# Kernel optimization log

Hardware: AMD Instinct MI355X
Metric: run time of the kernel (lower is better)

The kernel has to match this reference:

```python
import jax, jax.numpy as jnp
import numpy as np

D = 512
F = 2048
H = 8
L = 128
B = 4


def _layer_norm(x, g, b, eps=1e-5):
    mu = jnp.mean(x, axis=-1, keepdims=True)
    var = jnp.var(x, axis=-1, keepdims=True)
    return (x - mu) * jax.lax.rsqrt(var + eps) * g + b


def _edge_mlp(Q, arc, W, b, arc_is_middle_out):
    # Equivalent to relu(Linear(concat(A, arc, B_))) with W: (3D, D), without
    # materializing the (B,L,L,3D) concat: split W into three D-blocks.
    # For W_out: concat(h_bf, arc, h_bf_t) -> block1 acts on Q[b,i], block3 on Q[b,j].
    # For W_in:  concat(h_bf_t, arc, h_bf) -> block1 acts on Q[b,j], block3 on Q[b,i].
    d = Q.shape[-1]
    W1, W2, W3 = W[:d], W[d:2 * d], W[2 * d:]
    mid = jnp.einsum('bijd,de->bije', arc, W2)
    if arc_is_middle_out:  # W_out ordering
        left = jnp.einsum('bid,de->bie', Q, W1)[:, :, None, :]   # broadcast over j
        right = jnp.einsum('bjd,de->bje', Q, W3)[:, None, :, :]  # broadcast over i
    else:  # W_in ordering
        left = jnp.einsum('bjd,de->bje', Q, W1)[:, None, :, :]
        right = jnp.einsum('bid,de->bie', Q, W3)[:, :, None, :]
    return jax.nn.relu(left + mid + right + b)


def _gat_attn(Q, KV, q_w, q_b, k_w, k_b, v_w, v_b, o_w, o_b):
    # Edge-conditioned multihead attention: per-query K/V of shape (B,L,L,D).
    bsz, seq, d = Q.shape
    dh = d // H
    scale = dh ** -0.5
    q = ((Q @ q_w + q_b) * scale).reshape(bsz, seq, H, dh)
    k = (KV @ k_w + k_b).reshape(bsz, seq, seq, H, dh)
    v = (KV @ v_w + v_b).reshape(bsz, seq, seq, H, dh)
    scores = jnp.einsum('bihd,bijhd->bhij', q, k)
    attn = jax.nn.softmax(scores, axis=-1)
    out = jnp.einsum('bhij,bijhd->bihd', attn, v).reshape(bsz, seq, d)
    return out @ o_w + o_b


def setup_inputs() -> dict:
    key = jax.random.key(0)
    ks = jax.random.split(key, 24)
    s = 0.02
    inp = {
        'h': jax.random.normal(ks[0], (L, B, D), jnp.float32),
        'src_outcoming_arc_x': jax.random.normal(ks[1], (B, L, L, D), jnp.float32),
        'src_incoming_arc_x': jax.random.normal(ks[2], (B, L, L, D), jnp.float32),
        'encoder_padding_mask': jnp.zeros((B, L), jnp.bool_),
        'W_out_w': jax.random.normal(ks[3], (3 * D, D), jnp.float32) * s,
        'W_out_b': jnp.zeros((D,), jnp.float32),
        'W_in_w': jax.random.normal(ks[4], (3 * D, D), jnp.float32) * s,
        'W_in_b': jnp.zeros((D,), jnp.float32),
        'q_w': jax.random.normal(ks[5], (D, D), jnp.float32) * s,
        'q_b': jnp.zeros((D,), jnp.float32),
        'k_w': jax.random.normal(ks[6], (D, D), jnp.float32) * s,
        'k_b': jnp.zeros((D,), jnp.float32),
        'v_w': jax.random.normal(ks[7], (D, D), jnp.float32) * s,
        'v_b': jnp.zeros((D,), jnp.float32),
        'o_w': jax.random.normal(ks[8], (D, D), jnp.float32) * s,
        'o_b': jnp.zeros((D,), jnp.float32),
        'ln1_g': jnp.ones((D,), jnp.float32),
        'ln1_b': jnp.zeros((D,), jnp.float32),
        'fc1_w': jax.random.normal(ks[9], (D, F), jnp.float32) * s,
        'fc1_b': jnp.zeros((F,), jnp.float32),
        'fc2_w': jax.random.normal(ks[10], (F, D), jnp.float32) * s,
        'fc2_b': jnp.zeros((D,), jnp.float32),
        'ln2_g': jnp.ones((D,), jnp.float32),
        'ln2_b': jnp.zeros((D,), jnp.float32),
    }
    return inp


def reference(h, src_outcoming_arc_x, src_incoming_arc_x, encoder_padding_mask,
              W_out_w, W_out_b, W_in_w, W_in_b,
              q_w, q_b, k_w, k_b, v_w, v_b, o_w, o_b,
              ln1_g, ln1_b, fc1_w, fc1_b, fc2_w, fc2_b, ln2_g, ln2_b):
    # h: (L, B, D). Dropouts are identity (eval). attn_mask=None.
    residual = h
    Q = jnp.transpose(h, (1, 0, 2))  # (B, L, D)
    U_out = _edge_mlp(Q, src_outcoming_arc_x, W_out_w, W_out_b, True)
    att_out = _gat_attn(Q, U_out, q_w, q_b, k_w, k_b, v_w, v_b, o_w, o_b)
    U_in = _edge_mlp(Q, src_incoming_arc_x, W_in_w, W_in_b, False)
    att_in = _gat_attn(Q, U_in, q_w, q_b, k_w, k_b, v_w, v_b, o_w, o_b)
    x = jnp.transpose(att_in + att_out, (1, 0, 2))  # back to (L, B, D)
    x = _layer_norm(residual + x, ln1_g, ln1_b)
    residual = x
    x = jax.nn.relu(x @ fc1_w + fc1_b) @ fc2_w + fc2_b
    x = _layer_norm(residual + x, ln2_g, ln2_b)
    return x
```

## Files before the change

### kernel.cpp

```cpp
#include <hip/hip_runtime.h>
#include <stdint.h>
#include <stddef.h>

#define NTOK 512
#define NM   65536

typedef __bf16 bf16x8 __attribute__((ext_vector_type(8)));
typedef float  f32x4  __attribute__((ext_vector_type(4)));
typedef unsigned int u32x4 __attribute__((ext_vector_type(4)));

__device__ __forceinline__ unsigned short f2bf(float f) {
    unsigned int u = __builtin_bit_cast(unsigned int, f);
    u += 0x7FFFu + ((u >> 16) & 1u);
    return (unsigned short)(u >> 16);
}
__device__ __forceinline__ float bf2f(unsigned short s) {
    unsigned int u = ((unsigned int)s) << 16;
    return __builtin_bit_cast(float, u);
}

__device__ __forceinline__ void gload16(const void* g, void* l) {
    __builtin_amdgcn_global_load_lds(
        (const __attribute__((address_space(1))) void*)g,
        (__attribute__((address_space(3))) void*)l,
        16, 0, 0);
}

__global__ __launch_bounds__(256) void k_prep(const float* __restrict__ h,
                                              unsigned short* __restrict__ Qm,
                                              const float* __restrict__ kw,
                                              float* __restrict__ kwT,
                                              const float* __restrict__ Wob,
                                              const float* __restrict__ Wib,
                                              const float* __restrict__ qb,
                                              float* __restrict__ bias1) {
    int bid = blockIdx.x;
    int t = threadIdx.x;
    if (bid < 1024) {
        int idx = bid * 256 + t;
        int tok = idx >> 9, d = idx & 511;
        int b = tok >> 7, i = tok & 127;
        Qm[idx] = f2bf(h[(i * 4 + b) * 512 + d]);
    } else if (bid < 2048) {
        int idx = (bid - 1024) * 256 + t;
        kwT[idx] = kw[(size_t)(idx & 511) * 512 + (idx >> 9)];
    } else {
        int i = (bid - 2048) * 256 + t;
        if (i < 2560) {
            float v = 0.f;
            if (i < 512) v = Wob[i];
            else if (i < 1024) v = 0.f;
            else if (i < 1536) v = Wib[i - 1024];
            else if (i < 2048) v = 0.f;
            else v = qb[i - 2048] * 0.125f;
            bias1[i] = v;
        }
    }
}

struct TRJob { const float* src; unsigned short* dst; int srcLd, dstLd, tcols; float scale; };
struct TRJobs { TRJob j[11]; int start[12]; };

__global__ __launch_bounds__(256) void k_trN(TRJobs js) {
    __shared__ float tile[64][65];
    int b = blockIdx.x;
    int ji = 0;
    while (ji < 10 && b >= js.start[ji + 1]) ++ji;
    TRJob jb = js.j[ji];
    int rel = b - js.start[ji];
    int bx = rel % jb.tcols, by = rel / jb.tcols;
    int r0 = by * 64, c0 = bx * 64;
    int t = threadIdx.x;
    int c = t & 63, rr = t >> 6;
    #pragma unroll
    for (int ii = 0; ii < 16; ++ii) {
        int r = ii * 4 + rr;
        tile[r][c] = jb.src[(size_t)(r0 + r) * jb.srcLd + c0 + c];
    }
    __syncthreads();
    #pragma unroll
    for (int ii = 0; ii < 16; ++ii) {
        int n = ii * 4 + rr;
        jb.dst[(size_t)(c0 + n) * jb.dstLd + r0 + c] = f2bf(tile[c][n] * jb.scale);
    }
}

struct MMP {
    const unsigned short* A;  int lda;
    const unsigned short* Bt; int ldb;
    const float* bias;
    const float* accs;
    float* outF;
    unsigned short* outB;
    int ldo;
    int K;
    int relu;
    int aOffPerN64;
    int zKOff;
    int zOutOff;
    float biasScale;
};

__global__ __launch_bounds__(256) void k_mm(MMP p) {
    __shared__ unsigned char As[64 * 128];
    __shared__ unsigned char Bs[64 * 128];
    int t = threadIdx.x;
    int lane = t & 63, w = t >> 6;
    int m0 = blockIdx.x * 64, n0 = blockIdx.y * 64;
    int z = blockIdx.z;
    const unsigned short* A  = p.A + (size_t)(n0 >> 6) * p.aOffPerN64 + (size_t)z * p.zKOff;
    const unsigned short* Bt = p.Bt + (size_t)z * p.zKOff;
    int wm = (w >> 1) * 32, wn = (w & 1) * 32;
    f32x4 acc[2][2];
    #pragma unroll
    for (int a = 0; a < 2; ++a)
        #pragma unroll
        for (int b = 0; b < 2; ++b) acc[a][b] = (f32x4){0.f, 0.f, 0.f, 0.f};

    for (int kb = 0; kb < p.K; kb += 64) {
        __syncthreads();
        #pragma unroll
        for (int s = 0; s < 2; ++s) {
            int c = t + s * 256;
            int r = c >> 3, kc = (c & 7) * 8;
            int off = (r * 128 + kc * 2) ^ ((r & 7) << 4);
            *reinterpret_cast<u32x4*>(As + off) =
                *reinterpret_cast<const u32x4*>(A + (size_t)(m0 + r) * p.lda + kb + kc);
            *reinterpret_cast<u32x4*>(Bs + off) =
                *reinterpret_cast<const u32x4*>(Bt + (size_t)(n0 + r) * p.ldb + kb + kc);
        }
        __syncthreads();
        #pragma unroll
        for (int kh = 0; kh < 2; ++kh) {
            int kk = kh * 32 + (lane >> 4) * 8;
            bf16x8 af[2], bfr[2];
            #pragma unroll
            for (int mf = 0; mf < 2; ++mf) {
                int r = wm + mf * 16 + (lane & 15);
                int off = (r * 128 + kk * 2) ^ ((r & 7) << 4);
                af[mf] = *reinterpret_cast<const bf16x8*>(As + off);
            }
            #pragma unroll
            for (int nf = 0; nf < 2; ++nf) {
                int r = wn + nf * 16 + (lane & 15);
                int off = (r * 128 + kk * 2) ^ ((r & 7) << 4);
                bfr[nf] = *reinterpret_cast<const bf16x8*>(Bs + off);
            }
            #pragma unroll
            for (int mf = 0; mf < 2; ++mf)
                #pragma unroll
                for (int nf = 0; nf < 2; ++nf)
                    acc[mf][nf] = __builtin_amdgcn_mfma_f32_16x16x32_bf16(
                        af[mf], bfr[nf], acc[mf][nf], 0, 0, 0);
        }
    }
    #pragma unroll
    for (int mf = 0; mf < 2; ++mf) {
        #pragma unroll
        for (int rr = 0; rr < 4; ++rr) {
            int gm = m0 + wm + mf * 16 + (lane >> 4) * 4 + rr;
            #pragma unroll
            for (int nf = 0; nf < 2; ++nf) {
                int e = n0 + wn + nf * 16 + (lane & 15);
                float v = acc[mf][nf][rr];
                if (p.bias) v += p.bias[e] * p.biasScale;
                if (p.relu) v = fmaxf(v, 0.f);
                if (p.accs) v += p.accs[(size_t)gm * p.ldo + e];
                size_t oo = (size_t)gm * p.ldo + e + (size_t)z * p.zOutOff;
                if (p.outF) p.outF[oo] = v;
                if (p.outB) p.outB[oo] = f2bf(v);
            }
        }
    }
}

__global__ __launch_bounds__(256) void k_prep2(const float* __restrict__ qs, int qld,
                                               const float* __restrict__ kwT,
                                               const float* __restrict__ k_b,
                                               unsigned short* __restrict__ p,
                                               float* __restrict__ c) {
    __shared__ float q8[8][512];
    int t = threadIdx.x;
    int tok0 = blockIdx.x * 8;
    int d = blockIdx.y * 256 + t;
    for (int idx = t; idx < 4096; idx += 256) {
        int s = idx >> 9, dd = idx & 511;
        q8[s][dd] = qs[(size_t)(tok0 + s) * qld + dd];
    }
    __syncthreads();
    if (blockIdx.y == 0 && t < 64) {
        int s = t >> 3, hh = t & 7;
        float cv = 0.f;
        for (int dh = 0; dh < 64; ++dh) cv += k_b[hh * 64 + dh] * q8[s][hh * 64 + dh];
        c[(tok0 + s) * 8 + hh] = cv;
    }
    for (int hh = 0; hh < 8; ++hh) {
        float pv[8];
        #pragma unroll
        for (int s = 0; s < 8; ++s) pv[s] = 0.f;
        for (int dh = 0; dh < 64; ++dh) {
            float wv = kwT[(size_t)(hh * 64 + dh) * 512 + d];
            #pragma unroll
            for (int s = 0; s < 8; ++s) pv[s] += wv * q8[s][hh * 64 + dh];
        }
        #pragma unroll
        for (int s = 0; s < 8; ++s)
            p[((size_t)(tok0 + s) * 8 + hh) * 512 + d] = f2bf(pv[s]);
    }
}

__global__ __launch_bounds__(256) void k_midU(const float* __restrict__ arc,
                                              const unsigned short* __restrict__ W2t,
                                              const float* __restrict__ fixedMat, int fld,
                                              const float* __restrict__ rowMat, int rld,
                                              unsigned short* __restrict__ U) {
    __shared__ float As4[128 * 64];
    __shared__ unsigned short Bs2[128 * 64];
    int t = threadIdx.x;
    int lane = t & 63;
    int w = t >> 6;
    int bid = blockIdx.x;
    int xcd = bid & 7, slot = bid >> 3;
    int mt = xcd * 64 + (slot >> 2);
    int nt = slot & 3;
    int m0 = mt * 128;
    int n0 = nt * 128;
    int wm = (w >> 1) * 64, wn = (w & 1) * 64;
    f32x4 acc[4][4];
    #pragma unroll
    for (int a = 0; a < 4; ++a)
        #pragma unroll
        for (int bq = 0; bq < 4; ++bq) acc[a][bq] = (f32x4){0.f, 0.f, 0.f, 0.f};

    int arA = lane >> 4;
    int acb = lane & 15;
    int brB = lane >> 3;
    int bcb = lane & 7;

    for (int kb8 = 0; kb8 < 8; ++kb8) {
        int kb = kb8 * 64;
        __syncthreads();
        #pragma unroll
        for (int i = 0; i < 8; ++i) {
            int base = (w * 8 + i) * 1024;
            int r = ((w * 8 + i) << 2) + arA;
            int cs = acb ^ (r & 7);
            gload16(arc + (size_t)(m0 + r) * 512 + kb + cs * 4,
                    (char*)As4 + base);
        }
        #pragma unroll
        for (int i = 0; i < 4; ++i) {
            int base = (w * 4 + i) * 1024;
            int r = ((w * 4 + i) << 3) + brB;
            int cs = bcb ^ (r & 7);
            gload16(W2t + (size_t)(n0 + r) * 512 + kb + cs * 8,
                    (char*)Bs2 + base);
        }
        __syncthreads();
        #pragma unroll
        for (int kh = 0; kh < 2; ++kh) {
            int kk = kh * 32 + (lane >> 4) * 8;
            bf16x8 af[4], bfr[4];
            #pragma unroll
            for (int mf = 0; mf < 4; ++mf) {
                int rr = wm + mf * 16 + (lane & 15);
                int c0 = kk >> 2;
                const char* bp = (const char*)As4 + rr * 256;
                float4 a0 = *reinterpret_cast<const float4*>(bp + ((c0 ^ (rr & 7)) << 4));
                float4 a1 = *reinterpret_cast<const float4*>(bp + (((c0 + 1) ^ (rr & 7)) << 4));
                af[mf][0] = (__bf16)a0.x; af[mf][1] = (__bf16)a0.y;
                af[mf][2] = (__bf16)a0.z; af[mf][3] = (__bf16)a0.w;
                af[mf][4] = (__bf16)a1.x; af[mf][5] = (__bf16)a1.y;
                af[mf][6] = (__bf16)a1.z; af[mf][7] = (__bf16)a1.w;
            }
            #pragma unroll
            for (int nf = 0; nf < 4; ++nf) {
                int rn = wn + nf * 16 + (lane & 15);
                int c = kk >> 3;
                bfr[nf] = *reinterpret_cast<const bf16x8*>(
                    (const char*)Bs2 + rn * 128 + ((c ^ (rn & 7)) << 4));
            }
            #pragma unroll
            for (int mf = 0; mf < 4; ++mf)
                #pragma unroll
                for (int nf = 0; nf < 4; ++nf)
                    acc[mf][nf] = __builtin_amdgcn_mfma_f32_16x16x32_bf16(
                        af[mf], bfr[nf], acc[mf][nf], 0, 0, 0);
        }
    }
    int tokI = mt;
    int bb = mt >> 7;
    float fx[4];
    #pragma unroll
    for (int nf = 0; nf < 4; ++nf)
        fx[nf] = fixedMat[(size_t)tokI * fld + n0 + wn + nf * 16 + (lane & 15)];
    #pragma unroll
    for (int mf = 0; mf < 4; ++mf) {
        #pragma unroll
        for (int r = 0; r < 4; ++r) {
            int row = wm + mf * 16 + (lane >> 4) * 4 + r;
            int gm = m0 + row;
            int tokJ = bb * 128 + (gm & 127);
            const float* rv = rowMat + (size_t)tokJ * rld;
            #pragma unroll
            for (int nf = 0; nf < 4; ++nf) {
                int e = n0 + wn + nf * 16 + (lane & 15);
                float v = acc[mf][nf][r] + fx[nf] + rv[e];
                v = fmaxf(v, 0.f);
                U[(size_t)gm * 512 + e] = f2bf(v);
            }
        }
    }
}

__global__ __launch_bounds__(256) void k_att2(const unsigned short* __restrict__ U,
                                              const unsigned short* __restrict__ p,
                                              const float* __restrict__ c,
                                              float* __restrict__ Wsum,
                                              unsigned short* __restrict__ Waccb,
                                              int accum) {
    __shared__ float at[8][128];
    int tok = blockIdx.x;
    int t = threadIdx.x;
    int w = t >> 6;
    int lane = t & 63;
    int hh = lane & 15;
    int kg = lane >> 4;
    bool hv = hh < 8;
    f32x4 acc[2];
    acc[0] = (f32x4){0.f, 0.f, 0.f, 0.f};
    acc[1] = (f32x4){0.f, 0.f, 0.f, 0.f};
    const unsigned short* Ub0 = U + (size_t)tok * 65536;
    const unsigned short* Ub = Ub0 + (size_t)(w * 32) * 512;
    const unsigned short* pb = p + ((size_t)tok * 8 + (hh & 7)) * 512;
    for (int ks = 0; ks < 16; ++ks) {
        int kcol = ks * 32 + kg * 8;
        u32x4 braw = (u32x4){0u, 0u, 0u, 0u};
        if (hv) braw = *reinterpret_cast<const u32x4*>(pb + kcol);
        bf16x8 bfrag = __builtin_bit_cast(bf16x8, braw);
        #pragma unroll
        for (int mf = 0; mf < 2; ++mf) {
            bf16x8 afrag = *reinterpret_cast<const bf16x8*>(
                Ub + (size_t)(mf * 16 + hh) * 512 + kcol);
            acc[mf] = __builtin_amdgcn_mfma_f32_16x16x32_bf16(afrag, bfrag, acc[mf], 0, 0, 0);
        }
    }
    if (hv) {
        float cval = c[tok * 8 + hh];
        #pragma unroll
        for (int mf = 0; mf < 2; ++mf)
            #pragma unroll
            for (int r = 0; r < 4; ++r)
                at[hh][w * 32 + mf * 16 + kg * 4 + r] = acc[mf][r] + cval;
    }
    __syncthreads();
    {
        int h2 = t >> 5, l32 = t & 31;
        float v0 = at[h2][l32], v1 = at[h2][l32 + 32],
              v2 = at[h2][l32 + 64], v3 = at[h2][l32 + 96];
        float mx = fmaxf(fmaxf(v0, v1), fmaxf(v2, v3));
        #pragma unroll
        for (int o = 16; o >= 1; o >>= 1) mx = fmaxf(mx, __shfl_xor(mx, o));
        float e0 = __expf(v0 - mx), e1 = __expf(v1 - mx),
              e2 = __expf(v2 - mx), e3 = __expf(v3 - mx);
        float sum = e0 + e1 + e2 + e3;
        #pragma unroll
        for (int o = 16; o >= 1; o >>= 1) sum += __shfl_xor(sum, o);
        float inv = 1.f / sum;
        at[h2][l32]      = e0 * inv;
        at[h2][l32 + 32] = e1 * inv;
        at[h2][l32 + 64] = e2 * inv;
        at[h2][l32 + 96] = e3 * inv;
    }
    __syncthreads();
    int d0 = t * 2;
    float a8[8][2];
    #pragma unroll
    for (int q = 0; q < 8; ++q) { a8[q][0] = 0.f; a8[q][1] = 0.f; }
    for (int j = 0; j < 128; ++j) {
        unsigned int uv = *reinterpret_cast<const unsigned int*>(Ub0 + (size_t)j * 512 + d0);
        float u0 = bf2f((unsigned short)(uv & 0xffffu));
        float u1 = bf2f((unsigned short)(uv >> 16));
        #pragma unroll
        for (int q = 0; q < 8; ++q) {
            float a = at[q][j];
            a8[q][0] += a * u0;
            a8[q][1] += a * u1;
        }
    }
    #pragma unroll
    for (int q = 0; q < 8; ++q) {
        size_t woff = ((size_t)tok * 8 + q) * 512 + d0;
        if (!accum) {
            Wsum[woff] = a8[q][0];
            Wsum[woff + 1] = a8[q][1];
        } else {
            float s0 = Wsum[woff] + a8[q][0];
            float s1 = Wsum[woff + 1] + a8[q][1];
            Waccb[woff] = f2bf(s0);
            Waccb[woff + 1] = f2bf(s1);
        }
    }
}

__global__ __launch_bounds__(256) void k_ln(const float* __restrict__ A,
                                            const float* __restrict__ Bv, int bswap,
                                            const float* __restrict__ parts,
                                            const float* __restrict__ pbias,
                                            const float* __restrict__ g,
                                            const float* __restrict__ bta,
                                            float* __restrict__ outF,
                                            unsigned short* __restrict__ outB) {
    int t = threadIdx.x;
    int tok = blockIdx.x;
    size_t aoff = (size_t)tok * 512;
    float b0, b1;
    if (parts) {
        b0 = parts[aoff + t] + parts[262144 + aoff + t] +
             parts[524288 + aoff + t] + parts[786432 + aoff + t] + pbias[t];
        b1 = parts[aoff + t + 256] + parts[262144 + aoff + t + 256] +
             parts[524288 + aoff + t + 256] + parts[786432 + aoff + t + 256] + pbias[t + 256];
    } else {
        size_t boff = aoff;
        if (bswap) { int i = tok >> 2, b = tok & 3; boff = (size_t)(b * 128 + i) * 512; }
        b0 = Bv[boff + t];
        b1 = Bv[boff + t + 256];
    }
    float v0 = A[aoff + t] + b0;
    float v1 = A[aoff + t + 256] + b1;
    float s = v0 + v1, q = v0 * v0 + v1 * v1;
    #pragma unroll
    for (int o = 32; o >= 1; o >>= 1) { s += __shfl_xor(s, o); q += __shfl_xor(q, o); }
    __shared__ float red[8];
    int w = t >> 6, lane = t & 63;
    if (lane == 0) { red[w] = s; red[4 + w] = q; }
    __syncthreads();
    float ts = red[0] + red[1] + red[2] + red[3];
    float tq = red[4] + red[5] + red[6] + red[7];
    float mean = ts * (1.f / 512.f);
    float var = tq * (1.f / 512.f) - mean * mean;
    float inv = rsqrtf(var + 1e-5f);
    float o0 = (v0 - mean) * inv * g[t] + bta[t];
    float o1 = (v1 - mean) * inv * g[t + 256] + bta[t + 256];
    outF[aoff + t] = o0;
    outF[aoff + t + 256] = o1;
    if (outB) { outB[aoff + t] = f2bf(o0); outB[aoff + t + 256] = f2bf(o1); }
}

extern "C" void kernel_launch(void* const* d_in, const int* in_sizes, int n_in,
                              void* d_out, int out_size, void* d_ws, size_t ws_size,
                              hipStream_t stream) {
    (void)in_sizes; (void)n_in; (void)out_size; (void)ws_size;
    const float* h       = (const float*)d_in[0];
    const float* arc_out = (const float*)d_in[1];
    const float* arc_in  = (const float*)d_in[2];
    const float* W_out_w = (const float*)d_in[4];
    const float* W_out_b = (const float*)d_in[5];
    const float* W_in_w  = (const float*)d_in[6];
    const float* W_in_b  = (const float*)d_in[7];
    const float* q_w  = (const float*)d_in[8];
    const float* q_b  = (const float*)d_in[9];
    const float* k_w  = (const float*)d_in[10];
    const float* k_b  = (const float*)d_in[11];
    const float* v_w  = (const float*)d_in[12];
    const float* v_b  = (const float*)d_in[13];
    const float* o_w  = (const float*)d_in[14];
    const float* o_b  = (const float*)d_in[15];
    const float* ln1_g = (const float*)d_in[16];
    const float* ln1_b = (const float*)d_in[17];
    const float* fc1_w = (const float*)d_in[18];
    const float* fc1_b = (const float*)d_in[19];
    const float* fc2_w = (const float*)d_in[20];
    const float* fc2_b = (const float*)d_in[21];
    const float* ln2_g = (const float*)d_in[22];
    const float* ln2_b = (const float*)d_in[23];
    float* out = (float*)d_out;

    char* wsb = (char*)d_ws;
    size_t off = 0;
    auto ALLOC = [&](size_t bytes) -> void* {
        void* ptr = wsb + off;
        off += (bytes + 255) & ~(size_t)255;
        return ptr;
    };
    unsigned short* WcatT = (unsigned short*)ALLOC((size_t)2560 * 512 * 2);
    unsigned short* W2to  = (unsigned short*)ALLOC(262144 * 2);
    unsigned short* W2ti  = (unsigned short*)ALLOC(262144 * 2);
    unsigned short* o_wT  = (unsigned short*)ALLOC(262144 * 2);
    unsigned short* v_wT  = (unsigned short*)ALLOC(262144 * 2);
    unsigned short* fc1T  = (unsigned short*)ALLOC((size_t)2048 * 512 * 2);
    unsigned short* fc2T  = (unsigned short*)ALLOC((size_t)512 * 2048 * 2);
    float* kwT   = (float*)ALLOC(262144 * 4);
    float* bias1 = (float*)ALLOC(2560 * 4);
    unsigned short* Qm = (unsigned short*)ALLOC(262144 * 2);
    float* QWcat = (float*)ALLOC((size_t)512 * 2560 * 4);
    unsigned short* pbuf = (unsigned short*)ALLOC((size_t)NTOK * 8 * 512 * 2);
    float* cbuf = (float*)ALLOC(NTOK * 8 * 4);
    unsigned short* Ubuf = (unsigned short*)ALLOC((size_t)NM * 512 * 2);
    float* Wsum = (float*)ALLOC((size_t)NTOK * 8 * 512 * 4);
    unsigned short* Waccb = (unsigned short*)ALLOC((size_t)NTOK * 8 * 512 * 2);
    unsigned short* tmpb  = (unsigned short*)ALLOC(262144 * 2);
    float* attsum = (float*)ALLOC(262144 * 4);
    float* x1  = (float*)ALLOC(262144 * 4);
    unsigned short* x1b = (unsigned short*)ALLOC(262144 * 2);
    unsigned short* ybb = (unsigned short*)ALLOC((size_t)NTOK * 2048 * 2);
    float* zparts = (float*)ALLOC((size_t)4 * 262144 * 4);

    k_prep<<<2058, 256, 0, stream>>>(h, Qm, k_w, kwT, W_out_b, W_in_b, q_b, bias1);

    {
        TRJobs js = {};
        auto SET = [&](int i, const float* s, int sld, unsigned short* d, int dld,
                       float sc, int tiles, int tcols) {
            js.j[i] = TRJob{s, d, sld, dld, tcols, sc};
            js.start[i + 1] = js.start[i] + tiles;
        };
        js.start[0] = 0;
        SET(0,  W_out_w,              512, WcatT,              512, 1.f,    64, 8);
        SET(1,  W_out_w + 1024 * 512, 512, WcatT + 512 * 512,  512, 1.f,    64, 8);
        SET(2,  W_in_w,               512, WcatT + 1024 * 512, 512, 1.f,    64, 8);
        SET(3,  W_in_w + 1024 * 512,  512, WcatT + 1536 * 512, 512, 1.f,    64, 8);
        SET(4,  q_w,                  512, WcatT + 2048 * 512, 512, 0.125f, 64, 8);
        SET(5,  W_out_w + 512 * 512,  512, W2to,               512, 1.f,    64, 8);
        SET(6,  W_in_w + 512 * 512,   512, W2ti,               512, 1.f,    64, 8);
        SET(7,  o_w,                  512, o_wT,               512, 1.f,    64, 8);
        SET(8,  v_w,                  512, v_wT,               512, 1.f,    64, 8);
        SET(9,  fc1_w,               2048, fc1T,               512, 1.f,   256, 32);
        SET(10, fc2_w,                512, fc2T,              2048, 1.f,   256, 8);
        k_trN<<<js.start[11], 256, 0, stream>>>(js);
    }

    {
        MMP m = {};
        m.A = Qm; m.lda = 512; m.Bt = WcatT; m.ldb = 512;
        m.bias = bias1; m.biasScale = 1.f;
        m.outF = QWcat; m.ldo = 2560; m.K = 512;
        k_mm<<<dim3(8, 40), 256, 0, stream>>>(m);
    }
    k_prep2<<<dim3(64, 2), 256, 0, stream>>>(QWcat + 2048, 2560, kwT, k_b, pbuf, cbuf);

    for (int arc = 0; arc < 2; ++arc) {
        const float* arcp = (arc == 0) ? arc_out : arc_in;
        const unsigned short* w2 = (arc == 0) ? W2to : W2ti;
        const float* fixedM = (arc == 0) ? QWcat + 0    : QWcat + 1536;
        const float* rowM   = (arc == 0) ? QWcat + 512  : QWcat + 1024;
        k_midU<<<2048, 256, 0, stream>>>(arcp, w2, fixedM, 2560, rowM, 2560, Ubuf);
        k_att2<<<512, 256, 0, stream>>>(Ubuf, pbuf, cbuf, Wsum, Waccb, arc);
    }

    {
        MMP m = {};
        m.A = Waccb; m.lda = 4096; m.aOffPerN64 = 512;
        m.Bt = v_wT; m.ldb = 512;
        m.bias = v_b; m.biasScale = 2.f;
        m.outB = tmpb; m.ldo = 512; m.K = 512;
        k_mm<<<dim3(8, 8), 256, 0, stream>>>(m);
    }
    {
        MMP m = {};
        m.A = tmpb; m.lda = 512; m.Bt = o_wT; m.ldb = 512;
        m.bias = o_b; m.biasScale = 2.f;
        m.outF = attsum; m.ldo = 512; m.K = 512;
        k_mm<<<dim3(8, 8), 256, 0, stream>>>(m);
    }

    k_ln<<<512, 256, 0, stream>>>(h, attsum, 1, nullptr, nullptr, ln1_g, ln1_b, x1, x1b);

    {
        MMP m = {};
        m.A = x1b; m.lda = 512; m.Bt = fc1T; m.ldb = 512;
        m.bias = fc1_b; m.biasScale = 1.f;
        m.relu = 1; m.outB = ybb; m.ldo = 2048; m.K = 512;
        k_mm<<<dim3(8, 32), 256, 0, stream>>>(m);
    }
    {
        MMP m = {};
        m.A = ybb; m.lda = 2048; m.Bt = fc2T; m.ldb = 2048;
        m.outF = zparts; m.ldo = 512; m.K = 512;
        m.zKOff = 512; m.zOutOff = 262144;
        k_mm<<<dim3(8, 8, 4), 256, 0, stream>>>(m);
    }
    k_ln<<<512, 256, 0, stream>>>(x1, nullptr, 0, zparts, fc2_b, ln2_g, ln2_b, out, nullptr);
}
```

Measured before the change: 342.3 us.

## Read arc operand directly from global and double-buffer W2 tiles in LDS

In the edge-MLP GEMM kernel, the fp32 arc operand is no longer staged through shared memory; each wave loads its rows straight from global memory into registers before converting to bf16. The W2 tile gets a two-slot LDS buffer so the next k-slice is prefetched while the current one feeds the MFMAs, and one barrier per iteration is removed. This cuts LDS use and synchronisation, but the two waves sharing an M range now both fetch the same arc rows, with narrow strided float4 accesses that may coalesce poorly on the largest input stream.

```diff
diff --git a/kernel.cpp b/kernel.cpp
--- a/kernel.cpp
+++ b/kernel.cpp
@@ -214,8 +214,7 @@
                                               const float* __restrict__ fixedMat, int fld,
                                               const float* __restrict__ rowMat, int rld,
                                               unsigned short* __restrict__ U) {
-    __shared__ float As4[128 * 64];
-    __shared__ unsigned short Bs2[128 * 64];
+    __shared__ unsigned short Bs2[2][128 * 64];
     int t = threadIdx.x;
     int lane = t & 63;
     int w = t >> 6;
@@ -223,8 +222,7 @@
     int xcd = bid & 7, slot = bid >> 3;
     int mt = xcd * 64 + (slot >> 2);
     int nt = slot & 3;
-    int m0 = mt * 128;
-    int n0 = nt * 128;
+    int m0 = mt * 128, n0 = nt * 128;
     int wm = (w >> 1) * 64, wn = (w & 1) * 64;
     f32x4 acc[4][4];
     #pragma unroll
@@ -232,42 +230,38 @@
         #pragma unroll
         for (int bq = 0; bq < 4; ++bq) acc[a][bq] = (f32x4){0.f, 0.f, 0.f, 0.f};
 
-    int arA = lane >> 4;
-    int acb = lane & 15;
     int brB = lane >> 3;
     int bcb = lane & 7;
 
+    const float* aRow[4];
+    #pragma unroll
+    for (int mf = 0; mf < 4; ++mf)
+        aRow[mf] = arc + (size_t)(m0 + wm + mf * 16 + (lane & 15)) * 512;
+
+#define ISSUEB(KB, BUF)                                                         \
+    _Pragma("unroll")                                                           \
+    for (int i = 0; i < 4; ++i) {                                               \
+        int base = (w * 4 + i) * 1024;                                          \
+        int r = ((w * 4 + i) << 3) + brB;                                       \
+        int cs = bcb ^ (r & 7);                                                 \
+        gload16(W2t + (size_t)(n0 + r) * 512 + (KB) + cs * 8,                   \
+                (char*)Bs2[BUF] + base);                                        \
+    }
+
+    ISSUEB(0, 0);
+    #pragma unroll
     for (int kb8 = 0; kb8 < 8; ++kb8) {
         int kb = kb8 * 64;
         __syncthreads();
-        #pragma unroll
-        for (int i = 0; i < 8; ++i) {
-            int base = (w * 8 + i) * 1024;
-            int r = ((w * 8 + i) << 2) + arA;
-            int cs = acb ^ (r & 7);
-            gload16(arc + (size_t)(m0 + r) * 512 + kb + cs * 4,
-                    (char*)As4 + base);
-        }
-        #pragma unroll
-        for (int i = 0; i < 4; ++i) {
-            int base = (w * 4 + i) * 1024;
-            int r = ((w * 4 + i) << 3) + brB;
-            int cs = bcb ^ (r & 7);
-            gload16(W2t + (size_t)(n0 + r) * 512 + kb + cs * 8,
-                    (char*)Bs2 + base);
-        }
-        __syncthreads();
+        if (kb8 < 7) { ISSUEB(kb + 64, (kb8 & 1) ^ 1); }
         #pragma unroll
         for (int kh = 0; kh < 2; ++kh) {
             int kk = kh * 32 + (lane >> 4) * 8;
             bf16x8 af[4], bfr[4];
             #pragma unroll
             for (int mf = 0; mf < 4; ++mf) {
-                int rr = wm + mf * 16 + (lane & 15);
-                int c0 = kk >> 2;
-                const char* bp = (const char*)As4 + rr * 256;
-                float4 a0 = *reinterpret_cast<const float4*>(bp + ((c0 ^ (rr & 7)) << 4));
-                float4 a1 = *reinterpret_cast<const float4*>(bp + (((c0 + 1) ^ (rr & 7)) << 4));
+                float4 a0 = *reinterpret_cast<const float4*>(aRow[mf] + kb + kk);
+                float4 a1 = *reinterpret_cast<const float4*>(aRow[mf] + kb + kk + 4);
                 af[mf][0] = (__bf16)a0.x; af[mf][1] = (__bf16)a0.y;
                 af[mf][2] = (__bf16)a0.z; af[mf][3] = (__bf16)a0.w;
                 af[mf][4] = (__bf16)a1.x; af[mf][5] = (__bf16)a1.y;
@@ -278,7 +272,7 @@
                 int rn = wn + nf * 16 + (lane & 15);
                 int c = kk >> 3;
                 bfr[nf] = *reinterpret_cast<const bf16x8*>(
-                    (const char*)Bs2 + rn * 128 + ((c ^ (rn & 7)) << 4));
+                    (const char*)Bs2[kb8 & 1] + rn * 128 + ((c ^ (rn & 7)) << 4));
             }
             #pragma unroll
             for (int mf = 0; mf < 4; ++mf)
@@ -288,6 +282,7 @@
                         af[mf], bfr[nf], acc[mf][nf], 0, 0, 0);
         }
     }
+#undef ISSUEB
     int tokI = mt;
     int bb = mt >> 7;
     float fx[4];
```

Measured after the change: 531.0 us. 1.55x slower.

## Batch both arc directions into single launches and merge prep kernels

Applied to the files above, without the earlier changes.

Merges the prep and transpose kernels into one launch. Processes the outgoing and incoming arc edge-MLP and attention in single launches with twice the grid, using separate U and Wsum buffers per direction instead of running them sequentially. The fp32 sum of the two Wsum buffers and its bf16 conversion move into the A-tile load of the following matmul. This removes launches and tail underutilisation, at the cost of an extra 64MB U buffer, a doubled Wsum footprint, and fp32 A reads in that matmul.

```diff
diff --git a/kernel.cpp b/kernel.cpp
--- a/kernel.cpp
+++ b/kernel.cpp
@@ -26,51 +26,48 @@
         16, 0, 0);
 }
 
-__global__ __launch_bounds__(256) void k_prep(const float* __restrict__ h,
-                                              unsigned short* __restrict__ Qm,
-                                              const float* __restrict__ kw,
-                                              float* __restrict__ kwT,
-                                              const float* __restrict__ Wob,
-                                              const float* __restrict__ Wib,
-                                              const float* __restrict__ qb,
-                                              float* __restrict__ bias1) {
+struct TRJob { const float* src; unsigned short* dst; int srcLd, dstLd, tcols; float scale; };
+struct PrepArgs {
+    const float* h; unsigned short* Qm;
+    const float* kw; float* kwT;
+    const float* Wob; const float* Wib; const float* qb; float* bias1;
+    TRJob j[11]; int start[12];
+};
+
+__global__ __launch_bounds__(256) void k_prepAll(PrepArgs a) {
+    __shared__ float tile[64][65];
     int bid = blockIdx.x;
     int t = threadIdx.x;
     if (bid < 1024) {
         int idx = bid * 256 + t;
         int tok = idx >> 9, d = idx & 511;
         int b = tok >> 7, i = tok & 127;
-        Qm[idx] = f2bf(h[(i * 4 + b) * 512 + d]);
+        a.Qm[idx] = f2bf(a.h[(i * 4 + b) * 512 + d]);
+        return;
     } else if (bid < 2048) {
         int idx = (bid - 1024) * 256 + t;
-        kwT[idx] = kw[(size_t)(idx & 511) * 512 + (idx >> 9)];
-    } else {
+        a.kwT[idx] = a.kw[(size_t)(idx & 511) * 512 + (idx >> 9)];
+        return;
+    } else if (bid < 2058) {
         int i = (bid - 2048) * 256 + t;
         if (i < 2560) {
             float v = 0.f;
-            if (i < 512) v = Wob[i];
+            if (i < 512) v = a.Wob[i];
             else if (i < 1024) v = 0.f;
-            else if (i < 1536) v = Wib[i - 1024];
+            else if (i < 1536) v = a.Wib[i - 1024];
             else if (i < 2048) v = 0.f;
-            else v = qb[i - 2048] * 0.125f;
-            bias1[i] = v;
-        }
-    }
-}
-
-struct TRJob { const float* src; unsigned short* dst; int srcLd, dstLd, tcols; float scale; };
-struct TRJobs { TRJob j[11]; int start[12]; };
-
-__global__ __launch_bounds__(256) void k_trN(TRJobs js) {
-    __shared__ float tile[64][65];
-    int b = blockIdx.x;
+            else v = a.qb[i - 2048] * 0.125f;
+            a.bias1[i] = v;
+        }
+        return;
+    }
+    int b = bid - 2058;
     int ji = 0;
-    while (ji < 10 && b >= js.start[ji + 1]) ++ji;
-    TRJob jb = js.j[ji];
-    int rel = b - js.start[ji];
+    while (ji < 10 && b >= a.start[ji + 1]) ++ji;
+    TRJob jb = a.j[ji];
+    int rel = b - a.start[ji];
     int bx = rel % jb.tcols, by = rel / jb.tcols;
     int r0 = by * 64, c0 = bx * 64;
-    int t = threadIdx.x;
     int c = t & 63, rr = t >> 6;
     #pragma unroll
     for (int ii = 0; ii < 16; ++ii) {
@@ -87,6 +84,7 @@
 
 struct MMP {
     const unsigned short* A;  int lda;
+    const float* Af2a; const float* Af2b; int ldaf;
     const unsigned short* Bt; int ldb;
     const float* bias;
     const float* accs;
@@ -108,7 +106,8 @@
     int lane = t & 63, w = t >> 6;
     int m0 = blockIdx.x * 64, n0 = blockIdx.y * 64;
     int z = blockIdx.z;
-    const unsigned short* A  = p.A + (size_t)(n0 >> 6) * p.aOffPerN64 + (size_t)z * p.zKOff;
+    size_t aoffel = (size_t)(n0 >> 6) * p.aOffPerN64 + (size_t)z * p.zKOff;
+    const unsigned short* A  = p.A + aoffel;
     const unsigned short* Bt = p.Bt + (size_t)z * p.zKOff;
     int wm = (w >> 1) * 32, wn = (w & 1) * 32;
     f32x4 acc[2][2];
@@ -124,8 +123,21 @@
             int c = t + s * 256;
             int r = c >> 3, kc = (c & 7) * 8;
             int off = (r * 128 + kc * 2) ^ ((r & 7) << 4);
-            *reinterpret_cast<u32x4*>(As + off) =
-                *reinterpret_cast<const u32x4*>(A + (size_t)(m0 + r) * p.lda + kb + kc);
+            if (p.Af2a) {
+                size_t ro = aoffel + (size_t)(m0 + r) * p.ldaf + kb + kc;
+                const float4* xa = reinterpret_cast<const float4*>(p.Af2a + ro);
+                const float4* ya = reinterpret_cast<const float4*>(p.Af2b + ro);
+                float4 x0 = xa[0], x1 = xa[1], y0 = ya[0], y1 = ya[1];
+                bf16x8 bv;
+                bv[0] = (__bf16)(x0.x + y0.x); bv[1] = (__bf16)(x0.y + y0.y);
+                bv[2] = (__bf16)(x0.z + y0.z); bv[3] = (__bf16)(x0.w + y0.w);
+                bv[4] = (__bf16)(x1.x + y1.x); bv[5] = (__bf16)(x1.y + y1.y);
+                bv[6] = (__bf16)(x1.z + y1.z); bv[7] = (__bf16)(x1.w + y1.w);
+                *reinterpret_cast<bf16x8*>(As + off) = bv;
+            } else {
+                *reinterpret_cast<u32x4*>(As + off) =
+                    *reinterpret_cast<const u32x4*>(A + (size_t)(m0 + r) * p.lda + kb + kc);
+            }
             *reinterpret_cast<u32x4*>(Bs + off) =
                 *reinterpret_cast<const u32x4*>(Bt + (size_t)(n0 + r) * p.ldb + kb + kc);
         }
@@ -209,11 +221,13 @@
     }
 }
 
-__global__ __launch_bounds__(256) void k_midU(const float* __restrict__ arc,
-                                              const unsigned short* __restrict__ W2t,
-                                              const float* __restrict__ fixedMat, int fld,
-                                              const float* __restrict__ rowMat, int rld,
-                                              unsigned short* __restrict__ U) {
+__global__ __launch_bounds__(256) void k_midU(const float* __restrict__ arcO,
+                                              const float* __restrict__ arcI,
+                                              const unsigned short* __restrict__ W2to,
+                                              const unsigned short* __restrict__ W2ti,
+                                              const float* __restrict__ QWcat,
+                                              unsigned short* __restrict__ U0,
+                                              unsigned short* __restrict__ U1) {
     __shared__ float As4[128 * 64];
     __shared__ unsigned short Bs2[128 * 64];
     int t = threadIdx.x;
@@ -221,8 +235,15 @@
     int w = t >> 6;
     int bid = blockIdx.x;
     int xcd = bid & 7, slot = bid >> 3;
-    int mt = xcd * 64 + (slot >> 2);
+    int mtf = xcd * 128 + (slot >> 2);
     int nt = slot & 3;
+    int arc01 = mtf >> 9;
+    int mt = mtf & 511;
+    const float* arc = arc01 ? arcI : arcO;
+    const unsigned short* W2t = arc01 ? W2ti : W2to;
+    const float* fixedMat = QWcat + (arc01 ? 1536 : 0);
+    const float* rowMat   = QWcat + (arc01 ? 1024 : 512);
+    unsigned short* U = arc01 ? U1 : U0;
     int m0 = mt * 128;
     int n0 = nt * 128;
     int wm = (w >> 1) * 64, wn = (w & 1) * 64;
@@ -293,7 +314,7 @@
     float fx[4];
     #pragma unroll
     for (int nf = 0; nf < 4; ++nf)
-        fx[nf] = fixedMat[(size_t)tokI * fld + n0 + wn + nf * 16 + (lane & 15)];
+        fx[nf] = fixedMat[(size_t)tokI * 2560 + n0 + wn + nf * 16 + (lane & 15)];
     #pragma unroll
     for (int mf = 0; mf < 4; ++mf) {
         #pragma unroll
@@ -301,7 +322,7 @@
             int row = wm + mf * 16 + (lane >> 4) * 4 + r;
             int gm = m0 + row;
             int tokJ = bb * 128 + (gm & 127);
-            const float* rv = rowMat + (size_t)tokJ * rld;
+            const float* rv = rowMat + (size_t)tokJ * 2560;
             #pragma unroll
             for (int nf = 0; nf < 4; ++nf) {
                 int e = n0 + wn + nf * 16 + (lane & 15);
@@ -313,14 +334,18 @@
     }
 }
 
-__global__ __launch_bounds__(256) void k_att2(const unsigned short* __restrict__ U,
+__global__ __launch_bounds__(256) void k_att2(const unsigned short* __restrict__ U0,
+                                              const unsigned short* __restrict__ U1,
                                               const unsigned short* __restrict__ p,
                                               const float* __restrict__ c,
-                                              float* __restrict__ Wsum,
-                                              unsigned short* __restrict__ Waccb,
-                                              int accum) {
+                                              float* __restrict__ Wsum0,
+                                              float* __restrict__ Wsum1) {
     __shared__ float at[8][128];
-    int tok = blockIdx.x;
+    int bid = blockIdx.x;
+    int arc01 = bid >> 9;
+    int tok = bid & 511;
+    const unsigned short* U = arc01 ? U1 : U0;
+    float* Ws = arc01 ? Wsum1 : Wsum0;
     int t = threadIdx.x;
     int w = t >> 6;
     int lane = t & 63;
@@ -391,15 +416,8 @@
     #pragma unroll
     for (int q = 0; q < 8; ++q) {
         size_t woff = ((size_t)tok * 8 + q) * 512 + d0;
-        if (!accum) {
-            Wsum[woff] = a8[q][0];
-            Wsum[woff + 1] = a8[q][1];
-        } else {
-            float s0 = Wsum[woff] + a8[q][0];
-            float s1 = Wsum[woff + 1] + a8[q][1];
-            Waccb[woff] = f2bf(s0);
-            Waccb[woff + 1] = f2bf(s1);
-        }
+        Ws[woff] = a8[q][0];
+        Ws[woff + 1] = a8[q][1];
     }
 }
 
@@ -496,9 +514,10 @@
     float* QWcat = (float*)ALLOC((size_t)512 * 2560 * 4);
     unsigned short* pbuf = (unsigned short*)ALLOC((size_t)NTOK * 8 * 512 * 2);
     float* cbuf = (float*)ALLOC(NTOK * 8 * 4);
-    unsigned short* Ubuf = (unsigned short*)ALLOC((size_t)NM * 512 * 2);
-    float* Wsum = (float*)ALLOC((size_t)NTOK * 8 * 512 * 4);
-    unsigned short* Waccb = (unsigned short*)ALLOC((size_t)NTOK * 8 * 512 * 2);
+    unsigned short* Ubuf0 = (unsigned short*)ALLOC((size_t)NM * 512 * 2);
+    unsigned short* Ubuf1 = (unsigned short*)ALLOC((size_t)NM * 512 * 2);
+    float* Wsum0 = (float*)ALLOC((size_t)NTOK * 8 * 512 * 4);
+    float* Wsum1 = (float*)ALLOC((size_t)NTOK * 8 * 512 * 4);
     unsigned short* tmpb  = (unsigned short*)ALLOC(262144 * 2);
     float* attsum = (float*)ALLOC(262144 * 4);
     float* x1  = (float*)ALLOC(262144 * 4);
@@ -506,16 +525,16 @@
     unsigned short* ybb = (unsigned short*)ALLOC((size_t)NTOK * 2048 * 2);
     float* zparts = (float*)ALLOC((size_t)4 * 262144 * 4);
 
-    k_prep<<<2058, 256, 0, stream>>>(h, Qm, k_w, kwT, W_out_b, W_in_b, q_b, bias1);
-
-    {
-        TRJobs js = {};
+    {
+        PrepArgs a = {};
+        a.h = h; a.Qm = Qm; a.kw = k_w; a.kwT = kwT;
+        a.Wob = W_out_b; a.Wib = W_in_b; a.qb = q_b; a.bias1 = bias1;
         auto SET = [&](int i, const float* s, int sld, unsigned short* d, int dld,
                        float sc, int tiles, int tcols) {
-            js.j[i] = TRJob{s, d, sld, dld, tcols, sc};
-            js.start[i + 1] = js.start[i] + tiles;
+            a.j[i] = TRJob{s, d, sld, dld, tcols, sc};
+            a.start[i + 1] = a.start[i] + tiles;
         };
-        js.start[0] = 0;
+        a.start[0] = 0;
         SET(0,  W_out_w,              512, WcatT,              512, 1.f,    64, 8);
         SET(1,  W_out_w + 1024 * 512, 512, WcatT + 512 * 512,  512, 1.f,    64, 8);
         SET(2,  W_in_w,               512, WcatT + 1024 * 512, 512, 1.f,    64, 8);
@@ -527,7 +546,7 @@
         SET(8,  v_w,                  512, v_wT,               512, 1.f,    64, 8);
         SET(9,  fc1_w,               2048, fc1T,               512, 1.f,   256, 32);
         SET(10, fc2_w,                512, fc2T,              2048, 1.f,   256, 8);
-        k_trN<<<js.start[11], 256, 0, stream>>>(js);
+        k_prepAll<<<2058 + a.start[11], 256, 0, stream>>>(a);
     }
 
     {
@@ -539,18 +558,13 @@
     }
     k_prep2<<<dim3(64, 2), 256, 0, stream>>>(QWcat + 2048, 2560, kwT, k_b, pbuf, cbuf);
 
-    for (int arc = 0; arc < 2; ++arc) {
-        const float* arcp = (arc == 0) ? arc_out : arc_in;
-        const unsigned short* w2 = (arc == 0) ? W2to : W2ti;
-        const float* fixedM = (arc == 0) ? QWcat + 0    : QWcat + 1536;
-        const float* rowM   = (arc == 0) ? QWcat + 512  : QWcat + 1024;
-        k_midU<<<2048, 256, 0, stream>>>(arcp, w2, fixedM, 2560, rowM, 2560, Ubuf);
-        k_att2<<<512, 256, 0, stream>>>(Ubuf, pbuf, cbuf, Wsum, Waccb, arc);
-    }
+    k_midU<<<4096, 256, 0, stream>>>(arc_out, arc_in, W2to, W2ti, QWcat, Ubuf0, Ubuf1);
+    k_att2<<<1024, 256, 0, stream>>>(Ubuf0, Ubuf1, pbuf, cbuf, Wsum0, Wsum1);
 
     {
         MMP m = {};
-        m.A = Waccb; m.lda = 4096; m.aOffPerN64 = 512;
+        m.Af2a = Wsum0; m.Af2b = Wsum1; m.ldaf = 4096; m.aOffPerN64 = 512;
+        m.A = (const unsigned short*)Wsum0;
         m.Bt = v_wT; m.ldb = 512;
         m.bias = v_b; m.biasScale = 2.f;
         m.outB = tmpb; m.ldo = 512; m.K = 512;
```

Result: no change. 344.9 us (+0.8%).
